# Performance work log

Measured on AMD Instinct MI355X. Metric: run time of the kernel, lower is better.

Reference implementation:

```python
import jax, jax.numpy as jnp
import numpy as np
from jax import lax

B, T, H, L, LAT, OUT, NH = 4096, 60, 512, 2, 128, 14, 4
EPS = 1e-5


def _ln(x, g, b):
    m = x.mean(-1, keepdims=True)
    v = ((x - m) ** 2).mean(-1, keepdims=True)
    return (x - m) / jnp.sqrt(v + EPS) * g + b


def setup_inputs() -> dict:
    key = jax.random.key(0)
    ks = jax.random.split(key, 24)
    f32 = jnp.float32
    def rn(k, shape, s=0.05):
        return jax.random.normal(k, shape, dtype=f32) * s
    return {
        'x': jax.random.normal(ks[0], (B, T, 17), dtype=f32),
        'conv1_w': rn(ks[1], (24, 9, 3)), 'conv1_b': rn(ks[2], (24,)),
        'bn1_g': jnp.ones(24, f32), 'bn1_b': jnp.zeros(24, f32),
        'bn1_rm': rn(ks[3], (24,), 0.1), 'bn1_rv': jnp.full((24,), 0.8, f32),
        'comp_w': rn(ks[4], (20, 8)), 'comp_b': rn(ks[5], (20,)),
        'proj_w': rn(ks[6], (H, 44)), 'proj_b': rn(ks[7], (H,)),
        'gates_w': rn(ks[8], (L, 5, H, 2 * H), 0.02), 'gates_b': rn(ks[9], (L, 5, H)),
        'retention': jnp.full((L, H), 0.9, f32),
        'expln_g': jnp.ones((L, H), f32), 'expln_b': jnp.zeros((L, H), f32),
        'ln_g': jnp.ones((L, H), f32), 'ln_b': jnp.zeros((L, H), f32),
        'attn_in_w': rn(ks[10], (3 * H, H), 0.02), 'attn_in_b': rn(ks[11], (3 * H,)),
        'attn_out_w': rn(ks[12], (H, H), 0.02), 'attn_out_b': rn(ks[13], (H,)),
        'bneck_w': rn(ks[14], (LAT, H)), 'bneck_b': rn(ks[15], (LAT,)),
        'bn2_g': jnp.ones(LAT, f32), 'bn2_b': jnp.zeros(LAT, f32),
        'bn2_rm': rn(ks[16], (LAT,), 0.1), 'bn2_rv': jnp.full((LAT,), 0.9, f32),
        'out_w': rn(ks[17], (OUT, LAT)), 'out_b': rn(ks[18], (OUT,)),
    }


def _forward(x, conv1_w, conv1_b, bn1_g, bn1_b, bn1_rm, bn1_rv, comp_w, comp_b,
             proj_w, proj_b, gates_w, gates_b, retention, expln_g, expln_b,
             ln_g, ln_b, attn_in_w, attn_in_b, attn_out_w, attn_out_b,
             bneck_w, bneck_b, bn2_g, bn2_b, bn2_rm, bn2_rv, out_w, out_b):
    bsz = x.shape[0]
    hd = proj_w.shape[0]
    nlayers = gates_w.shape[0]
    # --- conv branch on relative features (eval-mode BatchNorm) ---
    rel = x[:, :, :9].transpose(0, 2, 1)                      # [B,9,T]
    y = lax.conv_general_dilated(rel, conv1_w, (1,), [(1, 1)],
                                 dimension_numbers=('NCH', 'OIH', 'NCH'))
    y = jax.nn.relu(y + conv1_b[None, :, None])
    y = (y - bn1_rm[None, :, None]) / jnp.sqrt(bn1_rv + EPS)[None, :, None] \
        * bn1_g[None, :, None] + bn1_b[None, :, None]
    th = y.shape[2] // 2
    y = y[:, :, :th * 2].reshape(bsz, 24, th, 2).max(-1)      # MaxPool1d(2)
    rel_feat = y.transpose(0, 2, 1)                           # [B,30,24]
    # --- company embedding branch ---
    comp = jax.nn.relu(x[:, :30, 9:] @ comp_w.T + comp_b)     # [B,30,20]
    combined = jnp.concatenate([rel_feat, comp], -1) @ proj_w.T + proj_b  # [B,30,H]
    # --- stacked xLSTM over time ---
    h0 = jnp.zeros((nlayers, bsz, hd), x.dtype)
    c0 = jnp.zeros((nlayers, bsz, hd), x.dtype)
    def step(carry, x_t):
        h, c = carry
        inp = x_t
        hs, cs = [], []
        for l in range(nlayers):
            comb = jnp.concatenate([inp, h[l]], -1)           # [B,2H]
            g = jnp.einsum('bk,ghk->gbh', comb, gates_w[l]) + gates_b[l][:, None, :]
            f = jax.nn.sigmoid(g[0]); i = jax.nn.sigmoid(g[1])
            o = jax.nn.sigmoid(g[2]); cc = jnp.tanh(g[3]); m = jax.nn.sigmoid(g[4])
            r = retention[l]
            c_new = f * c[l] + i * cc
            c_new = c_new * r + (1 - r) * c[l]
            c_new = m * c_new + (1 - m) * c[l]
            o_exp = jax.nn.sigmoid(_ln(o, expln_g[l], expln_b[l]))  # exp(z)/(1+exp(z))
            h_new = _ln(o_exp * jnp.tanh(c_new), ln_g[l], ln_b[l])
            hs.append(h_new); cs.append(c_new)
            inp = h_new
        return (jnp.stack(hs), jnp.stack(cs)), inp
    _, seq = lax.scan(step, (h0, c0), combined.transpose(1, 0, 2))
    seq = seq.transpose(1, 0, 2)                              # [B,30,H]
    # --- multi-head self attention (eval, 4 heads) ---
    dh = hd // NH
    qkv = seq @ attn_in_w.T + attn_in_b
    q, k, v = jnp.split(qkv, 3, axis=-1)
    q = q.reshape(bsz, -1, NH, dh); k = k.reshape(bsz, -1, NH, dh); v = v.reshape(bsz, -1, NH, dh)
    scores = jnp.einsum('bqhd,bkhd->bhqk', q, k) / jnp.sqrt(jnp.float32(dh))
    attn = jnp.einsum('bhqk,bkhd->bqhd', jax.nn.softmax(scores, -1), v)
    attn = attn.reshape(bsz, -1, hd) @ attn_out_w.T + attn_out_b
    final = attn[:, -1, :]
    latent = final @ bneck_w.T + bneck_b
    latent = (latent - bn2_rm) / jnp.sqrt(bn2_rv + EPS) * bn2_g + bn2_b
    return latent @ out_w.T + out_b


def reference(x, conv1_w, conv1_b, bn1_g, bn1_b, bn1_rm, bn1_rv, comp_w, comp_b,
              proj_w, proj_b, gates_w, gates_b, retention, expln_g, expln_b,
              ln_g, ln_b, attn_in_w, attn_in_b, attn_out_w, attn_out_b,
              bneck_w, bneck_b, bn2_g, bn2_b, bn2_rm, bn2_rv, out_w, out_b):
    return _forward(x, conv1_w, conv1_b, bn1_g, bn1_b, bn1_rm, bn1_rv, comp_w, comp_b,
                    proj_w, proj_b, gates_w, gates_b, retention, expln_g, expln_b,
                    ln_g, ln_b, attn_in_w, attn_in_b, attn_out_w, attn_out_b,
                    bneck_w, bneck_b, bn2_g, bn2_b, bn2_rm, bn2_rv, out_w, out_b)
```

## Files before the change

kernel.cpp:

```cpp
#include <hip/hip_runtime.h>
#include <hip/hip_bf16.h>

#define B_   4096
#define T_   60
#define TT   30
#define H_   512
#define L_   2
#define NH_  4
#define DH_  128
#define LAT_ 128
#define OUT_ 14
#define NGATE_ (5*H_)
#define EPSF 1e-5f
#define FEATK 64

typedef __attribute__((ext_vector_type(8))) short bf16x8;
typedef __attribute__((ext_vector_type(4))) float f32x4;

__device__ __forceinline__ float sigmoidf_(float x) { return 1.0f / (1.0f + __expf(-x)); }
__device__ __forceinline__ float bf2f(short s) {
    return __uint_as_float(((unsigned)(unsigned short)s) << 16);
}

__device__ __forceinline__ void async_load16(const void* g, void* l) {
    __builtin_amdgcn_global_load_lds((const __attribute__((address_space(1))) void*)g,
                                     (__attribute__((address_space(3))) void*)l, 16, 0, 0);
}

__global__ __launch_bounds__(256) void cvt_bf16(const float* __restrict__ in,
                                                __hip_bfloat16* __restrict__ out, long n) {
    long i = (long)blockIdx.x * blockDim.x + threadIdx.x;
    long stride = (long)gridDim.x * blockDim.x;
    for (; i < n; i += stride) out[i] = __float2bfloat16(in[i]);
}

__global__ __launch_bounds__(256) void zero_f32(float* __restrict__ p, long n) {
    long i = (long)blockIdx.x * blockDim.x + threadIdx.x;
    long stride = (long)gridDim.x * blockDim.x;
    for (; i < n; i += stride) p[i] = 0.0f;
}

__global__ __launch_bounds__(256) void pad_projw(const float* __restrict__ pw,
                                                 __hip_bfloat16* __restrict__ out) {
    int i = blockIdx.x * 256 + threadIdx.x;
    if (i >= H_ * FEATK) return;
    int r = i >> 6, c = i & 63;
    out[i] = __float2bfloat16(c < 44 ? pw[r * 44 + c] : 0.f);
}

__global__ __launch_bounds__(256)
void build_wkd(const float* __restrict__ aiw, __hip_bfloat16* __restrict__ wkd) {
    int i = blockIdx.x * 256 + threadIdx.x;
    if (i >= 2048 * 512) return;
    int n = i >> 9, k = i & 511;
    float v = ((k >> 7) == (n >> 9)) ? aiw[(H_ + k) * H_ + (n & 511)] : 0.f;
    wkd[i] = __float2bfloat16(v);
}

__global__ __launch_bounds__(256)
void build_wvd(const float* __restrict__ aiw, __hip_bfloat16* __restrict__ wvd) {
    int i = blockIdx.x * 256 + threadIdx.x;
    if (i >= 512 * 2048) return;
    int n = i >> 11, k = i & 2047;
    float v = ((k >> 9) == (n >> 7)) ? aiw[(2 * H_ + n) * H_ + (k & 511)] : 0.f;
    wvd[i] = __float2bfloat16(v);
}

__global__ __launch_bounds__(256)
void frontend_kernel(const float* __restrict__ x,
                     const float* __restrict__ cw, const float* __restrict__ cb,
                     const float* __restrict__ bg, const float* __restrict__ bb,
                     const float* __restrict__ brm, const float* __restrict__ brv,
                     const float* __restrict__ compw, const float* __restrict__ compb,
                     __hip_bfloat16* __restrict__ feat_out) {
    const int b = blockIdx.x, tid = threadIdx.x;
    __shared__ float xs[T_ * 17];
    __shared__ float ybuf[24][T_];
    __shared__ float feat[TT][44];

    for (int i = tid; i < T_ * 17; i += 256) xs[i] = x[(long)b * T_ * 17 + i];
    __syncthreads();

    for (int i = tid; i < 24 * T_; i += 256) {
        int oc = i / T_, t = i % T_;
        float acc = cb[oc];
        #pragma unroll
        for (int kk = 0; kk < 3; ++kk) {
            int tt = t + kk - 1;
            if (tt >= 0 && tt < T_) {
                #pragma unroll
                for (int ic = 0; ic < 9; ++ic)
                    acc += xs[tt * 17 + ic] * cw[(oc * 9 + ic) * 3 + kk];
            }
        }
        acc = fmaxf(acc, 0.f);
        acc = (acc - brm[oc]) * rsqrtf(brv[oc] + EPSF) * bg[oc] + bb[oc];
        ybuf[oc][t] = acc;
    }
    __syncthreads();

    for (int i = tid; i < TT * 24; i += 256) {
        int u = i / 24, oc = i % 24;
        feat[u][oc] = fmaxf(ybuf[oc][2 * u], ybuf[oc][2 * u + 1]);
    }
    for (int i = tid; i < TT * 20; i += 256) {
        int u = i / 20, oc = i % 20;
        float acc = compb[oc];
        #pragma unroll
        for (int j = 0; j < 8; ++j) acc += xs[u * 17 + 9 + j] * compw[oc * 8 + j];
        feat[u][24 + oc] = fmaxf(acc, 0.f);
    }
    __syncthreads();

    for (int i = tid; i < TT * FEATK; i += 256) {
        int u = i >> 6, c = i & 63;
        float v = (c < 44) ? feat[u][c] : 0.f;
        feat_out[((long)b * TT + u) * FEATK + c] = __float2bfloat16(v);
    }
}

template <int WRITE_BF16>
__device__ __forceinline__
void gemm_core(const __hip_bfloat16* __restrict__ A0, int lda0,
               const __hip_bfloat16* __restrict__ A1, int lda1, int ksplit,
               const __hip_bfloat16* __restrict__ W, int ldw,
               const float* __restrict__ bias,
               void* __restrict__ Cout, int ldc, int K, int bx, int by) {
    __shared__ __hip_bfloat16 As[128 * 64];
    __shared__ __hip_bfloat16 Bs[128 * 64];
    const int tid = threadIdx.x;
    const int wave = tid >> 6, lane = tid & 63;
    const long m0 = (long)by * 128;
    const long n0 = (long)bx * 128;

    f32x4 acc[4][4] = {};

    for (int k0 = 0; k0 < K; k0 += 64) {
        __syncthreads();
        #pragma unroll
        for (int it = 0; it < 4; ++it) {
            int id = it * 256 + tid;
            int row = id >> 3;
            int kc = ((id & 7) ^ (row & 7)) << 3;
            int gk = k0 + kc;
            const __hip_bfloat16* srcA;
            if (gk < ksplit) srcA = A0 + (m0 + row) * (long)lda0 + gk;
            else             srcA = A1 + (m0 + row) * (long)lda1 + (gk - ksplit);
            async_load16(srcA, &As[id * 8]);
            const __hip_bfloat16* srcB = W + (n0 + row) * (long)ldw + gk;
            async_load16(srcB, &Bs[id * 8]);
        }
        __syncthreads();
        #pragma unroll
        for (int ks = 0; ks < 2; ++ks) {
            const int kb = ((ks * 4 + (lane >> 4)) ^ (lane & 7)) << 3;
            const int ar = (wave >> 1) * 64 + (lane & 15);
            const int br = (wave & 1) * 64 + (lane & 15);
            bf16x8 afr[4], bfr[4];
            #pragma unroll
            for (int i = 0; i < 4; ++i) afr[i] = *(const bf16x8*)&As[(ar + i * 16) * 64 + kb];
            #pragma unroll
            for (int i = 0; i < 4; ++i) bfr[i] = *(const bf16x8*)&Bs[(br + i * 16) * 64 + kb];
            #pragma unroll
            for (int mi = 0; mi < 4; ++mi)
                #pragma unroll
                for (int ni = 0; ni < 4; ++ni)
                    acc[mi][ni] = __builtin_amdgcn_mfma_f32_16x16x32_bf16(afr[mi], bfr[ni], acc[mi][ni], 0, 0, 0);
        }
    }

    const int cr = (lane >> 4) * 4;
    const int ccol = lane & 15;
    #pragma unroll
    for (int ni = 0; ni < 4; ++ni) {
        long col = n0 + (wave & 1) * 64 + ni * 16 + ccol;
        float bv = bias ? bias[col] : 0.f;
        #pragma unroll
        for (int mi = 0; mi < 4; ++mi) {
            long rowb = m0 + (wave >> 1) * 64 + mi * 16 + cr;
            #pragma unroll
            for (int r = 0; r < 4; ++r) {
                float v = acc[mi][ni][r] + bv;
                if (WRITE_BF16)
                    ((__hip_bfloat16*)Cout)[(rowb + r) * (long)ldc + col] = __float2bfloat16(v);
                else
                    ((float*)Cout)[(rowb + r) * (long)ldc + col] = v;
            }
        }
    }
}

template <int WRITE_BF16>
__global__ __launch_bounds__(256)
void gemm_bias(const __hip_bfloat16* __restrict__ A0, int lda0,
               const __hip_bfloat16* __restrict__ A1, int lda1, int ksplit,
               const __hip_bfloat16* __restrict__ W, int ldw,
               const float* __restrict__ bias,
               void* __restrict__ Cout, int ldc, int K) {
    gemm_core<WRITE_BF16>(A0, lda0, A1, lda1, ksplit, W, ldw, bias, Cout, ldc, K,
                          blockIdx.x, blockIdx.y);
}

template <int WRITE_BF16>
__global__ __launch_bounds__(256)
void gemm_dual_db(const __hip_bfloat16* A0a, int lda0a, const __hip_bfloat16* A1a,
                  int lda1a, int Ka, const __hip_bfloat16* Wa,
                  const float* biasa, void* Ca,
                  const __hip_bfloat16* A0b, int lda0b, const __hip_bfloat16* A1b,
                  int lda1b, int Kb, const __hip_bfloat16* Wb,
                  const float* biasb, void* Cb,
                  int ksplit, int ldw, int ldc) {
    const int id = blockIdx.x;
    const int xcd = id & 7;
    const int mhalf = xcd >> 2;
    const int czg = xcd & 3;
    const int rest = id >> 3;
    const int m = mhalf * 16 + (rest & 15);
    const int colz = czg * 10 + (rest >> 4);
    const int col = colz % 20;
    const int z = colz / 20;
    const __hip_bfloat16* A0 = z ? A0b : A0a;
    const __hip_bfloat16* A1 = z ? A1b : A1a;
    const __hip_bfloat16* W  = z ? Wb  : Wa;
    const float* bias        = z ? biasb : biasa;
    void* Cout               = z ? Cb : Ca;
    int lda0 = z ? lda0b : lda0a;
    int lda1 = z ? lda1b : lda1a;
    int K    = z ? Kb : Ka;

    __shared__ __hip_bfloat16 As[2][128 * 32];
    __shared__ __hip_bfloat16 Bs[2][128 * 32];
    const int tid = threadIdx.x;
    const int wave = tid >> 6, lane = tid & 63;
    const long m0 = (long)m * 128;
    const long n0 = (long)col * 128;

    f32x4 acc[4][4] = {};

    auto stage = [&](int hb, int k0) {
        #pragma unroll
        for (int it = 0; it < 2; ++it) {
            int sid = it * 256 + tid;
            int row = sid >> 2;
            int kc = ((sid & 3) ^ ((row >> 1) & 3)) << 3;
            int gk = k0 + kc;
            const __hip_bfloat16* srcA;
            if (gk < ksplit) srcA = A0 + (m0 + row) * (long)lda0 + gk;
            else             srcA = A1 + (m0 + row) * (long)lda1 + (gk - ksplit);
            async_load16(srcA, &As[hb][sid * 8]);
            const __hip_bfloat16* srcB = W + (n0 + row) * (long)ldw + gk;
            async_load16(srcB, &Bs[hb][sid * 8]);
        }
    };

    stage(0, 0);
    const int nslab = K >> 5;
    const int kb = ((lane >> 4) ^ ((lane >> 1) & 3)) << 3;
    const int ar = (wave >> 1) * 64 + (lane & 15);
    const int br = (wave & 1) * 64 + (lane & 15);

    for (int kk = 0; kk < nslab; ++kk) {
        const int hb = kk & 1;
        __syncthreads();
        if (kk + 1 < nslab) stage(hb ^ 1, (kk + 1) << 5);
        bf16x8 afr[4], bfr[4];
        #pragma unroll
        for (int i = 0; i < 4; ++i) afr[i] = *(const bf16x8*)&As[hb][(ar + i * 16) * 32 + kb];
        #pragma unroll
        for (int i = 0; i < 4; ++i) bfr[i] = *(const bf16x8*)&Bs[hb][(br + i * 16) * 32 + kb];
        #pragma unroll
        for (int mi = 0; mi < 4; ++mi)
            #pragma unroll
            for (int ni = 0; ni < 4; ++ni)
                acc[mi][ni] = __builtin_amdgcn_mfma_f32_16x16x32_bf16(afr[mi], bfr[ni], acc[mi][ni], 0, 0, 0);
    }

    const int cr = (lane >> 4) * 4;
    const int ccol = lane & 15;
    #pragma unroll
    for (int ni = 0; ni < 4; ++ni) {
        long ccol2 = n0 + (wave & 1) * 64 + ni * 16 + ccol;
        float bv = bias ? bias[ccol2] : 0.f;
        #pragma unroll
        for (int mi = 0; mi < 4; ++mi) {
            long rowb = m0 + (wave >> 1) * 64 + mi * 16 + cr;
            #pragma unroll
            for (int r = 0; r < 4; ++r) {
                float v = acc[mi][ni][r] + bv;
                if (WRITE_BF16)
                    ((__hip_bfloat16*)Cout)[(rowb + r) * (long)ldc + ccol2] = __float2bfloat16(v);
                else
                    ((float*)Cout)[(rowb + r) * (long)ldc + ccol2] = v;
            }
        }
    }
}

__device__ __forceinline__ void block_reduce2(float& a, float& b, float* red) {
    #pragma unroll
    for (int off = 32; off > 0; off >>= 1) {
        a += __shfl_down(a, off, 64);
        b += __shfl_down(b, off, 64);
    }
    int lane = threadIdx.x & 63, w = threadIdx.x >> 6;
    if (lane == 0) { red[w] = a; red[8 + w] = b; }
    __syncthreads();
    a = red[0] + red[1] + red[2] + red[3];
    b = red[8] + red[9] + red[10] + red[11];
    __syncthreads();
}

__device__ __forceinline__
void gate_ew_body(const __hip_bfloat16* __restrict__ g, float* __restrict__ c,
                  const float* __restrict__ ret,
                  const float* __restrict__ elg, const float* __restrict__ elb,
                  const float* __restrict__ lng, const float* __restrict__ lnb,
                  __hip_bfloat16* __restrict__ hout, long hstride, int b) {
    const int tid = threadIdx.x;
    const __hip_bfloat16* gr = g + (long)b * NGATE_;
    __shared__ float red[16];

    float o_[2], cn_[2];
    float s = 0.f, s2 = 0.f;
    #pragma unroll
    for (int u = 0; u < 2; ++u) {
        int j = tid + u * 256;
        float fg = __bfloat162float(gr[j]);
        float ig = __bfloat162float(gr[512 + j]);
        float og = __bfloat162float(gr[1024 + j]);
        float cg = __bfloat162float(gr[1536 + j]);
        float mg = __bfloat162float(gr[2048 + j]);
        float f = sigmoidf_(fg), i = sigmoidf_(ig), o = sigmoidf_(og);
        float cc = tanhf(cg), m = sigmoidf_(mg);
        float cold = c[(long)b * H_ + j];
        float r = ret[j];
        float cn = f * cold + i * cc;
        cn = cn * r + (1.f - r) * cold;
        cn = m * cn + (1.f - m) * cold;
        c[(long)b * H_ + j] = cn;
        o_[u] = o; cn_[u] = cn;
        s += o; s2 += o * o;
    }
    block_reduce2(s, s2, red);
    float mean = s * (1.f / H_);
    float var = s2 * (1.f / H_) - mean * mean;
    float rstd = rsqrtf(var + EPSF);

    float val[2];
    float s3 = 0.f, s4 = 0.f;
    #pragma unroll
    for (int u = 0; u < 2; ++u) {
        int j = tid + u * 256;
        float on = (o_[u] - mean) * rstd * elg[j] + elb[j];
        float oe = sigmoidf_(on);
        float v = oe * tanhf(cn_[u]);
        val[u] = v; s3 += v; s4 += v * v;
    }
    block_reduce2(s3, s4, red);
    float mean2 = s3 * (1.f / H_);
    float var2 = s4 * (1.f / H_) - mean2 * mean2;
    float rstd2 = rsqrtf(var2 + EPSF);
    #pragma unroll
    for (int u = 0; u < 2; ++u) {
        int j = tid + u * 256;
        float h = (val[u] - mean2) * rstd2 * lng[j] + lnb[j];
        hout[(long)b * hstride + j] = __float2bfloat16(h);
    }
}

__global__ __launch_bounds__(256)
void gate_ew(const __hip_bfloat16* __restrict__ g, float* __restrict__ c,
             const float* __restrict__ ret,
             const float* __restrict__ elg, const float* __restrict__ elb,
             const float* __restrict__ lng, const float* __restrict__ lnb,
             __hip_bfloat16* __restrict__ hout, long hstride) {
    gate_ew_body(g, c, ret, elg, elb, lng, lnb, hout, hstride, blockIdx.x);
}

__global__ __launch_bounds__(256)
void gate_ew_dual(const __hip_bfloat16* ga, float* ca, const float* reta,
                  const float* elga, const float* elba,
                  const float* lnga, const float* lnba,
                  __hip_bfloat16* houta, long hstridea,
                  const __hip_bfloat16* gb, float* cb, const float* retb,
                  const float* elgb, const float* elbb,
                  const float* lngb, const float* lnbb,
                  __hip_bfloat16* houtb, long hstrideb) {
    int bid = blockIdx.x;
    bool isB = bid >= B_;
    int b = isB ? bid - B_ : bid;
    const __hip_bfloat16* g = isB ? gb : ga;
    float* c        = isB ? cb : ca;
    const float* ret = isB ? retb : reta;
    const float* elg = isB ? elgb : elga;
    const float* elb = isB ? elbb : elba;
    const float* lng = isB ? lngb : lnga;
    const float* lnb = isB ? lnbb : lnba;
    __hip_bfloat16* hout = isB ? houtb : houta;
    long hstride = isB ? hstrideb : hstridea;
    gate_ew_body(g, c, ret, elg, elb, lng, lnb, hout, hstride, b);
}

__global__ __launch_bounds__(256)
void attn_fused(const __hip_bfloat16* __restrict__ seq,
                const __hip_bfloat16* __restrict__ U,
                __hip_bfloat16* __restrict__ sbar) {
    const int b = blockIdx.x, tid = threadIdx.x;
    const int h = tid >> 6, lane = tid & 63;
    const int c0 = lane * 8;
    __shared__ float ps[NH_ * TT];
    const float scale = 0.08838834764831845f;

    float uq[8];
    {
        bf16x8 uv = *(const bf16x8*)&U[(size_t)b * (NH_ * H_) + h * H_ + c0];
        for (int j = 0; j < 8; ++j) uq[j] = bf2f(uv[j]);
    }
    const __hip_bfloat16* srow = seq + (size_t)b * TT * H_;

    for (int t = 0; t < TT; ++t) {
        bf16x8 sv = *(const bf16x8*)&srow[t * H_ + c0];
        float a = 0.f;
        for (int j = 0; j < 8; ++j) a += uq[j] * bf2f(sv[j]);
        a += __shfl_xor(a, 32);
        a += __shfl_xor(a, 16);
        a += __shfl_xor(a, 8);
        a += __shfl_xor(a, 4);
        a += __shfl_xor(a, 2);
        a += __shfl_xor(a, 1);
        if (lane == 0) ps[h * TT + t] = a * scale;
    }
    __syncthreads();

    float mx = -1e30f;
    for (int t = 0; t < TT; ++t) mx = fmaxf(mx, ps[h * TT + t]);
    float den = 0.f;
    for (int t = 0; t < TT; ++t) den += __expf(ps[h * TT + t] - mx);
    float inv = 1.f / den;

    float accv[8];
    for (int j = 0; j < 8; ++j) accv[j] = 0.f;
    for (int t = 0; t < TT; ++t) {
        float w = __expf(ps[h * TT + t] - mx) * inv;
        bf16x8 sv = *(const bf16x8*)&srow[t * H_ + c0];
        for (int j = 0; j < 8; ++j) accv[j] += w * bf2f(sv[j]);
    }
    bf16x8 outv;
    for (int j = 0; j < 8; ++j) {
        __hip_bfloat16 hv = __float2bfloat16(accv[j]);
        outv[j] = *(short*)&hv;
    }
    *(bf16x8*)&sbar[(size_t)b * (NH_ * H_) + h * H_ + c0] = outv;
}

__global__ __launch_bounds__(128)
void head_kernel(const float* __restrict__ lat_in,
                 const float* __restrict__ g2, const float* __restrict__ b2,
                 const float* __restrict__ rm2, const float* __restrict__ rv2,
                 const float* __restrict__ ow, const float* __restrict__ ob,
                 float* __restrict__ out) {
    const int b = blockIdx.x, tid = threadIdx.x;
    __shared__ float ls[LAT_];
    float a = lat_in[(long)b * LAT_ + tid];
    ls[tid] = (a - rm2[tid]) * rsqrtf(rv2[tid] + EPSF) * g2[tid] + b2[tid];
    __syncthreads();
    if (tid < OUT_) {
        float acc = ob[tid];
        #pragma unroll 4
        for (int j = 0; j < LAT_; ++j) acc += ls[j] * ow[tid * LAT_ + j];
        out[(long)b * OUT_ + tid] = acc;
    }
}

extern "C" void kernel_launch(void* const* d_in, const int* in_sizes, int n_in,
                              void* d_out, int out_size, void* d_ws, size_t ws_size,
                              hipStream_t stream) {
    const float* x        = (const float*)d_in[0];
    const float* conv1_w  = (const float*)d_in[1];
    const float* conv1_b  = (const float*)d_in[2];
    const float* bn1_g    = (const float*)d_in[3];
    const float* bn1_b    = (const float*)d_in[4];
    const float* bn1_rm   = (const float*)d_in[5];
    const float* bn1_rv   = (const float*)d_in[6];
    const float* comp_w   = (const float*)d_in[7];
    const float* comp_b   = (const float*)d_in[8];
    const float* proj_w   = (const float*)d_in[9];
    const float* proj_b   = (const float*)d_in[10];
    const float* gates_w  = (const float*)d_in[11];
    const float* gates_b  = (const float*)d_in[12];
    const float* retention= (const float*)d_in[13];
    const float* expln_g  = (const float*)d_in[14];
    const float* expln_b  = (const float*)d_in[15];
    const float* ln_g     = (const float*)d_in[16];
    const float* ln_b     = (const float*)d_in[17];
    const float* attn_in_w  = (const float*)d_in[18];
    const float* attn_in_b  = (const float*)d_in[19];
    const float* attn_out_w = (const float*)d_in[20];
    const float* attn_out_b = (const float*)d_in[21];
    const float* bneck_w  = (const float*)d_in[22];
    const float* bneck_b  = (const float*)d_in[23];
    const float* bn2_g    = (const float*)d_in[24];
    const float* bn2_b    = (const float*)d_in[25];
    const float* bn2_rm   = (const float*)d_in[26];
    const float* bn2_rv   = (const float*)d_in[27];
    const float* out_w    = (const float*)d_in[28];
    const float* out_b    = (const float*)d_in[29];
    float* out = (float*)d_out;

    char* base = (char*)d_ws;
    size_t off = 0;
    auto alloc = [&](size_t nbytes) -> char* {
        char* p = base + off;
        off += (nbytes + 255) & ~(size_t)255;
        return p;
    };
    __hip_bfloat16* seq_bf = (__hip_bfloat16*)alloc((size_t)B_ * TT * H_ * 2);
    size_t g_bytes = (size_t)B_ * NGATE_ * 2;
    char* un = alloc(2 * g_bytes);
    __hip_bfloat16* feat_bf = (__hip_bfloat16*)un;
    __hip_bfloat16* gA_bf   = (__hip_bfloat16*)un;
    __hip_bfloat16* gB_bf   = (__hip_bfloat16*)(un + g_bytes);
    __hip_bfloat16* U_bf    = (__hip_bfloat16*)un;
    __hip_bfloat16* sbar_bf = (__hip_bfloat16*)(un + (size_t)16 * 1024 * 1024);
    __hip_bfloat16* wkd_bf  = (__hip_bfloat16*)(un + (size_t)32 * 1024 * 1024);
    __hip_bfloat16* wvd_bf  = (__hip_bfloat16*)(un + (size_t)35 * 1024 * 1024);
    float*          c0    = (float*)alloc((size_t)B_ * H_ * 4);
    float*          c1    = (float*)alloc((size_t)B_ * H_ * 4);
    __hip_bfloat16* h0_bf = (__hip_bfloat16*)alloc((size_t)B_ * H_ * 2);
    __hip_bfloat16* q_bf  = (__hip_bfloat16*)alloc((size_t)B_ * H_ * 2);
    __hip_bfloat16* fin_bf = q_bf;
    __hip_bfloat16* av_bf = (__hip_bfloat16*)alloc((size_t)B_ * H_ * 2);
    float*          lat_f = (float*)alloc((size_t)B_ * LAT_ * 4);
    __hip_bfloat16* gw_bf = (__hip_bfloat16*)alloc((size_t)L_ * 5 * H_ * 2 * H_ * 2);
    __hip_bfloat16* ai_bf = (__hip_bfloat16*)alloc((size_t)H_ * H_ * 2);
    __hip_bfloat16* ao_bf = (__hip_bfloat16*)alloc((size_t)H_ * H_ * 2);
    __hip_bfloat16* pw_bf = (__hip_bfloat16*)alloc((size_t)H_ * FEATK * 2);
    __hip_bfloat16* bw_bf = (__hip_bfloat16*)alloc((size_t)LAT_ * H_ * 2);
    (void)ws_size; (void)in_sizes; (void)n_in; (void)out_size;

    cvt_bf16<<<2048, 256, 0, stream>>>(gates_w, gw_bf, (long)L_ * 5 * H_ * 2 * H_);
    cvt_bf16<<<256, 256, 0, stream>>>(attn_in_w, ai_bf, (long)H_ * H_);
    cvt_bf16<<<256, 256, 0, stream>>>(attn_out_w, ao_bf, (long)H_ * H_);
    cvt_bf16<<<64, 256, 0, stream>>>(bneck_w, bw_bf, (long)LAT_ * H_);
    pad_projw<<<(H_ * FEATK + 255) / 256, 256, 0, stream>>>(proj_w, pw_bf);
    zero_f32<<<2048, 256, 0, stream>>>(c0, (long)2 * B_ * H_);

    frontend_kernel<<<B_, 256, 0, stream>>>(x, conv1_w, conv1_b, bn1_g, bn1_b, bn1_rm,
                                            bn1_rv, comp_w, comp_b, feat_bf);
    gemm_bias<1><<<dim3(H_ / 128, (B_ * TT) / 128), 256, 0, stream>>>(
        feat_bf, FEATK, (const __hip_bfloat16*)nullptr, 0, FEATK,
        pw_bf, FEATK, proj_b, (void*)seq_bf, H_, FEATK);

    const int WL = 5 * H_ * 2 * H_;
    const dim3 ggrid(NGATE_ / 128, B_ / 128);

    gemm_bias<1><<<ggrid, 256, 0, stream>>>(
        seq_bf, TT * H_, (const __hip_bfloat16*)nullptr, 0, H_,
        gw_bf, 2 * H_, gates_b, (void*)gB_bf, NGATE_, H_);
    gate_ew<<<B_, 256, 0, stream>>>(gB_bf, c0, retention, expln_g, expln_b,
                                    ln_g, ln_b, h0_bf, H_);

    for (int t = 0; t < TT - 1; ++t) {
        gemm_dual_db<1><<<1280, 256, 0, stream>>>(
            h0_bf, H_, (t == 0) ? (const __hip_bfloat16*)nullptr
                                : seq_bf + (size_t)(t - 1) * H_,
            TT * H_, (t == 0) ? H_ : 2 * H_, gw_bf + WL, gates_b + NGATE_, (void*)gA_bf,
            seq_bf + (size_t)(t + 1) * H_, TT * H_, h0_bf, H_, 2 * H_,
            gw_bf, gates_b, (void*)gB_bf,
            H_, 2 * H_, NGATE_);
        gate_ew_dual<<<2 * B_, 256, 0, stream>>>(
            gA_bf, c1, retention + H_, expln_g + H_, expln_b + H_,
            ln_g + H_, ln_b + H_, seq_bf + (size_t)t * H_, TT * H_,
            gB_bf, c0, retention, expln_g, expln_b,
            ln_g, ln_b, h0_bf, H_);
    }
    gemm_bias<1><<<ggrid, 256, 0, stream>>>(
        h0_bf, H_, seq_bf + (size_t)(TT - 2) * H_, TT * H_, H_,
        gw_bf + WL, 2 * H_, gates_b + NGATE_, (void*)gA_bf, NGATE_, 2 * H_);
    gate_ew<<<B_, 256, 0, stream>>>(gA_bf, c1, retention + H_, expln_g + H_,
                                    expln_b + H_, ln_g + H_, ln_b + H_,
                                    seq_bf + (size_t)(TT - 1) * H_, TT * H_);

    build_wkd<<<4096, 256, 0, stream>>>(attn_in_w, wkd_bf);
    build_wvd<<<4096, 256, 0, stream>>>(attn_in_w, wvd_bf);

    gemm_bias<1><<<dim3(H_ / 128, B_ / 128), 256, 0, stream>>>(
        seq_bf + (size_t)29 * H_, TT * H_, (const __hip_bfloat16*)nullptr, 0, H_,
        ai_bf, H_, attn_in_b, (void*)q_bf, H_, H_);

    gemm_bias<1><<<dim3(2048 / 128, B_ / 128), 256, 0, stream>>>(
        q_bf, H_, (const __hip_bfloat16*)nullptr, 0, H_,
        wkd_bf, H_, (const float*)nullptr, (void*)U_bf, 2048, H_);

    attn_fused<<<B_, 256, 0, stream>>>(seq_bf, U_bf, sbar_bf);

    gemm_bias<1><<<dim3(H_ / 128, B_ / 128), 256, 0, stream>>>(
        sbar_bf, 2048, (const __hip_bfloat16*)nullptr, 0, 2048,
        wvd_bf, 2048, attn_in_b + 2 * H_, (void*)av_bf, H_, 2048);

    gemm_bias<1><<<dim3(H_ / 128, B_ / 128), 256, 0, stream>>>(
        av_bf, H_, (const __hip_bfloat16*)nullptr, 0, H_,
        ao_bf, H_, attn_out_b, (void*)fin_bf, H_, H_);

    gemm_bias<0><<<dim3(LAT_ / 128, B_ / 128), 256, 0, stream>>>(
        fin_bf, H_, (const __hip_bfloat16*)nullptr, 0, H_,
        bw_bf, H_, bneck_b, (void*)lat_f, LAT_, H_);
    head_kernel<<<B_, 128, 0, stream>>>(lat_f, bn2_g, bn2_b, bn2_rm, bn2_rv,
                                        out_w, out_b, out);
}
```

Measured before the change: 2.820 ms.

## Fold input projection into layer-0 gate weights, shrinking per-step K

Precomputes W0·proj_w (and a folded bias) so layer-0 gates read the 64-wide padded features directly instead of the 512-wide projected sequence. This removes the large projection GEMM and cuts the layer-0 input-side K from 512 to 64 in every timestep GEMM. The combined weight is built on the device in fp32 with a simple per-thread dot loop. Rounding changes because the product is now formed before the bf16 cast.

Measured after the change: 2.755 ms. 1.02x faster.

```diff
diff --git a/kernel.cpp b/kernel.cpp
--- a/kernel.cpp
+++ b/kernel.cpp
@@ -13,6 +13,7 @@
 #define NGATE_ (5*H_)
 #define EPSF 1e-5f
 #define FEATK 64
+#define K0M  (FEATK + H_)
 
 typedef __attribute__((ext_vector_type(8))) short bf16x8;
 typedef __attribute__((ext_vector_type(4))) float f32x4;
@@ -40,12 +41,30 @@
     for (; i < n; i += stride) p[i] = 0.0f;
 }
 
-__global__ __launch_bounds__(256) void pad_projw(const float* __restrict__ pw,
-                                                 __hip_bfloat16* __restrict__ out) {
-    int i = blockIdx.x * 256 + threadIdx.x;
-    if (i >= H_ * FEATK) return;
-    int r = i >> 6, c = i & 63;
-    out[i] = __float2bfloat16(c < 44 ? pw[r * 44 + c] : 0.f);
+__global__ __launch_bounds__(256)
+void build_w0m(const float* __restrict__ gw, const float* __restrict__ pw,
+               const float* __restrict__ pb, const float* __restrict__ gb,
+               __hip_bfloat16* __restrict__ w0m, float* __restrict__ bc) {
+    const int tid = threadIdx.x;
+    const int n = blockIdx.x * 4 + (tid >> 6);
+    const int f = tid & 63;
+    const float* wrow = gw + (long)n * (2 * H_);
+    float acc = 0.f;
+    if (f < 44) {
+        for (int k = 0; k < H_; ++k) acc += wrow[k] * pw[k * 44 + f];
+    }
+    w0m[(long)n * K0M + f] = __float2bfloat16(acc);
+    #pragma unroll
+    for (int j = 0; j < 8; ++j) {
+        int col = f * 8 + j;
+        w0m[(long)n * K0M + FEATK + col] = __float2bfloat16(wrow[H_ + col]);
+    }
+    float s = 0.f;
+    #pragma unroll
+    for (int j = 0; j < 8; ++j) s += wrow[f * 8 + j] * pb[f * 8 + j];
+    #pragma unroll
+    for (int off = 32; off > 0; off >>= 1) s += __shfl_down(s, off, 64);
+    if (f == 0) bc[n] = gb[n] + s;
 }
 
 __global__ __launch_bounds__(256)
@@ -205,11 +224,11 @@
 __global__ __launch_bounds__(256)
 void gemm_dual_db(const __hip_bfloat16* A0a, int lda0a, const __hip_bfloat16* A1a,
                   int lda1a, int Ka, const __hip_bfloat16* Wa,
-                  const float* biasa, void* Ca,
+                  const float* biasa, void* Ca, int ksplita, int ldwa,
                   const __hip_bfloat16* A0b, int lda0b, const __hip_bfloat16* A1b,
                   int lda1b, int Kb, const __hip_bfloat16* Wb,
-                  const float* biasb, void* Cb,
-                  int ksplit, int ldw, int ldc) {
+                  const float* biasb, void* Cb, int ksplitb, int ldwb,
+                  int ldc) {
     const int id = blockIdx.x;
     const int xcd = id & 7;
     const int mhalf = xcd >> 2;
@@ -227,6 +246,8 @@
     int lda0 = z ? lda0b : lda0a;
     int lda1 = z ? lda1b : lda1a;
     int K    = z ? Kb : Ka;
+    int ksplit = z ? ksplitb : ksplita;
+    int ldw    = z ? ldwb : ldwa;
 
     __shared__ __hip_bfloat16 As[2][128 * 32];
     __shared__ __hip_bfloat16 Bs[2][128 * 32];
@@ -517,13 +538,13 @@
     __hip_bfloat16* seq_bf = (__hip_bfloat16*)alloc((size_t)B_ * TT * H_ * 2);
     size_t g_bytes = (size_t)B_ * NGATE_ * 2;
     char* un = alloc(2 * g_bytes);
-    __hip_bfloat16* feat_bf = (__hip_bfloat16*)un;
     __hip_bfloat16* gA_bf   = (__hip_bfloat16*)un;
     __hip_bfloat16* gB_bf   = (__hip_bfloat16*)(un + g_bytes);
     __hip_bfloat16* U_bf    = (__hip_bfloat16*)un;
     __hip_bfloat16* sbar_bf = (__hip_bfloat16*)(un + (size_t)16 * 1024 * 1024);
     __hip_bfloat16* wkd_bf  = (__hip_bfloat16*)(un + (size_t)32 * 1024 * 1024);
     __hip_bfloat16* wvd_bf  = (__hip_bfloat16*)(un + (size_t)35 * 1024 * 1024);
+    __hip_bfloat16* feat_bf = (__hip_bfloat16*)alloc((size_t)B_ * TT * FEATK * 2);
     float*          c0    = (float*)alloc((size_t)B_ * H_ * 4);
     float*          c1    = (float*)alloc((size_t)B_ * H_ * 4);
     __hip_bfloat16* h0_bf = (__hip_bfloat16*)alloc((size_t)B_ * H_ * 2);
@@ -532,31 +553,30 @@
     __hip_bfloat16* av_bf = (__hip_bfloat16*)alloc((size_t)B_ * H_ * 2);
     float*          lat_f = (float*)alloc((size_t)B_ * LAT_ * 4);
     __hip_bfloat16* gw_bf = (__hip_bfloat16*)alloc((size_t)L_ * 5 * H_ * 2 * H_ * 2);
+    __hip_bfloat16* w0m_bf = (__hip_bfloat16*)alloc((size_t)NGATE_ * K0M * 2);
+    float*          bc_f  = (float*)alloc((size_t)NGATE_ * 4);
     __hip_bfloat16* ai_bf = (__hip_bfloat16*)alloc((size_t)H_ * H_ * 2);
     __hip_bfloat16* ao_bf = (__hip_bfloat16*)alloc((size_t)H_ * H_ * 2);
-    __hip_bfloat16* pw_bf = (__hip_bfloat16*)alloc((size_t)H_ * FEATK * 2);
     __hip_bfloat16* bw_bf = (__hip_bfloat16*)alloc((size_t)LAT_ * H_ * 2);
     (void)ws_size; (void)in_sizes; (void)n_in; (void)out_size;
 
-    cvt_bf16<<<2048, 256, 0, stream>>>(gates_w, gw_bf, (long)L_ * 5 * H_ * 2 * H_);
+    const int WL = 5 * H_ * 2 * H_;
+    cvt_bf16<<<1024, 256, 0, stream>>>(gates_w + WL, gw_bf + WL, (long)WL);
+    build_w0m<<<NGATE_ / 4, 256, 0, stream>>>(gates_w, proj_w, proj_b, gates_b,
+                                              w0m_bf, bc_f);
     cvt_bf16<<<256, 256, 0, stream>>>(attn_in_w, ai_bf, (long)H_ * H_);
     cvt_bf16<<<256, 256, 0, stream>>>(attn_out_w, ao_bf, (long)H_ * H_);
     cvt_bf16<<<64, 256, 0, stream>>>(bneck_w, bw_bf, (long)LAT_ * H_);
-    pad_projw<<<(H_ * FEATK + 255) / 256, 256, 0, stream>>>(proj_w, pw_bf);
     zero_f32<<<2048, 256, 0, stream>>>(c0, (long)2 * B_ * H_);
 
     frontend_kernel<<<B_, 256, 0, stream>>>(x, conv1_w, conv1_b, bn1_g, bn1_b, bn1_rm,
                                             bn1_rv, comp_w, comp_b, feat_bf);
-    gemm_bias<1><<<dim3(H_ / 128, (B_ * TT) / 128), 256, 0, stream>>>(
-        feat_bf, FEATK, (const __hip_bfloat16*)nullptr, 0, FEATK,
-        pw_bf, FEATK, proj_b, (void*)seq_bf, H_, FEATK);
-
-    const int WL = 5 * H_ * 2 * H_;
+
     const dim3 ggrid(NGATE_ / 128, B_ / 128);
 
     gemm_bias<1><<<ggrid, 256, 0, stream>>>(
-        seq_bf, TT * H_, (const __hip_bfloat16*)nullptr, 0, H_,
-        gw_bf, 2 * H_, gates_b, (void*)gB_bf, NGATE_, H_);
+        feat_bf, TT * FEATK, (const __hip_bfloat16*)nullptr, 0, FEATK,
+        w0m_bf, K0M, bc_f, (void*)gB_bf, NGATE_, FEATK);
     gate_ew<<<B_, 256, 0, stream>>>(gB_bf, c0, retention, expln_g, expln_b,
                                     ln_g, ln_b, h0_bf, H_);
 
@@ -565,9 +585,11 @@
             h0_bf, H_, (t == 0) ? (const __hip_bfloat16*)nullptr
                                 : seq_bf + (size_t)(t - 1) * H_,
             TT * H_, (t == 0) ? H_ : 2 * H_, gw_bf + WL, gates_b + NGATE_, (void*)gA_bf,
-            seq_bf + (size_t)(t + 1) * H_, TT * H_, h0_bf, H_, 2 * H_,
-            gw_bf, gates_b, (void*)gB_bf,
-            H_, 2 * H_, NGATE_);
+            H_, 2 * H_,
+            feat_bf + (size_t)(t + 1) * FEATK, TT * FEATK, h0_bf, H_, K0M,
+            w0m_bf, bc_f, (void*)gB_bf,
+            FEATK, K0M,
+            NGATE_);
         gate_ew_dual<<<2 * B_, 256, 0, stream>>>(
             gA_bf, c1, retention + H_, expln_g + H_, expln_b + H_,
             ln_g + H_, ln_b + H_, seq_bf + (size_t)t * H_, TT * H_,
```
